# Kernel tuning notes

Hardware: AMD Instinct MI355X
Metric: run time of the kernel (lower is better)

Reference implementation:

```python
import jax, jax.numpy as jnp
import numpy as np

N_PER_GRAPH = 1024
BATCH = 32
N = N_PER_GRAPH * BATCH  # 32768 total nodes
E = 262144               # edges per edge set (before self loops)
EMB = 128
D = 128
NEG_SLOPE = 0.2


def setup_inputs() -> dict:
    key = jax.random.key(0)
    ks = jax.random.split(key, 20)
    def lin(k, i, o):
        return (jax.random.normal(k, (i, o), jnp.float32) / np.float32(np.sqrt(i)))
    inp = {}
    inp["x"] = jax.random.normal(ks[0], (N, EMB), jnp.float32)
    inp["edge_index_n"] = jax.random.randint(ks[1], (2, E), 0, N, jnp.int32)
    inp["edge_index_r0"] = jax.random.randint(ks[2], (2, E), 0, N, jnp.int32)
    inp["edge_index_r1"] = jax.random.randint(ks[3], (2, E), 0, N, jnp.int32)
    # gat_0: Linear(EMB->D) + attn Linear(2D->D)
    inp["W0_lin"] = lin(ks[4], EMB, D); inp["b0_lin"] = jnp.zeros((D,), jnp.float32)
    inp["W0_att"] = lin(ks[5], 2 * D, D); inp["b0_att"] = jnp.zeros((D,), jnp.float32)
    # gat_1 (shared, used twice)
    inp["W1_lin"] = lin(ks[6], D, D); inp["b1_lin"] = jnp.zeros((D,), jnp.float32)
    inp["W1_att"] = lin(ks[7], 2 * D, D); inp["b1_att"] = jnp.zeros((D,), jnp.float32)
    # gat_2 (shared, used twice)
    inp["W2_lin"] = lin(ks[8], D, D); inp["b2_lin"] = jnp.zeros((D,), jnp.float32)
    inp["W2_att"] = lin(ks[9], 2 * D, D); inp["b2_att"] = jnp.zeros((D,), jnp.float32)
    # lin_prob: Linear(D->1)
    inp["Wp"] = lin(ks[10], D, 1); inp["bp"] = jnp.zeros((1,), jnp.float32)
    # Attention: W1, W2 (D->D, no bias), vt (D->1, no bias)
    inp["Wa1"] = lin(ks[11], D, D)
    inp["Wa2"] = lin(ks[12], D, D)
    inp["vt"] = lin(ks[13], D, 1)
    return inp


def _gat(x, edge_index, Wl, bl, Wa, ba):
    """One GATConv: add self loops, lin, edge gather, attn MLP, segment softmax, scatter-add."""
    n = x.shape[0]
    loop = jnp.arange(n, dtype=edge_index.dtype)
    src = jnp.concatenate([edge_index[0], loop])  # x_j index
    dst = jnp.concatenate([edge_index[1], loop])  # x_i / aggregation index
    h = x @ Wl + bl                               # [N, D]
    hi = h[dst]                                   # [E+N, D]
    hj = h[src]                                   # [E+N, D]
    a = jnp.concatenate([hi, hj], axis=-1) @ Wa + ba  # [E+N, D]
    a = jax.nn.leaky_relu(a, NEG_SLOPE)
    # segment softmax over destination neighborhoods (vector-valued, per channel)
    m = jax.lax.stop_gradient(jax.ops.segment_max(a, dst, num_segments=n))
    ex = jnp.exp(a - m[dst])
    s = jax.ops.segment_sum(ex, dst, num_segments=n)
    alpha = ex / (s[dst] + 1e-16)
    return jax.ops.segment_sum(hj * alpha, dst, num_segments=n)


def reference(x, edge_index_n, edge_index_r0, edge_index_r1,
              W0_lin, b0_lin, W0_att, b0_att,
              W1_lin, b1_lin, W1_att, b1_att,
              W2_lin, b2_lin, W2_att, b2_att,
              Wp, bp, Wa1, Wa2, vt):
    g0 = _gat(x,  edge_index_n,  W0_lin, b0_lin, W0_att, b0_att)
    g1 = _gat(g0, edge_index_r1, W1_lin, b1_lin, W1_att, b1_att)
    g2 = _gat(g1, edge_index_r0, W2_lin, b2_lin, W2_att, b2_att)
    g3 = _gat(g2, edge_index_r1, W1_lin, b1_lin, W1_att, b1_att)
    g4 = _gat(g3, edge_index_r0, W2_lin, b2_lin, W2_att, b2_att)
    X = g4.reshape(BATCH, N_PER_GRAPH, D)
    h = X.mean(axis=1)                                       # [B, D]
    logits1 = (X @ Wp + bp).reshape(BATCH, N_PER_GRAPH)      # [B, n]
    prob1 = jax.nn.softmax(logits1[:, 1:], axis=-1)          # [B, n-1]
    k1, k2 = jax.random.split(jax.random.key(42))
    index1 = 1 + jax.random.categorical(k1, logits1[:, 1:], axis=-1)  # [B]
    b_ar = jnp.arange(BATCH)
    sampled = X[b_ar, index1][:, None, :]                    # [B, 1, D]
    u = (jnp.tanh(sampled @ Wa1 + X @ Wa2) @ vt)[..., 0]      # [B, n]
    u = u.at[b_ar, index1].set(-jnp.inf)
    prob2 = jax.nn.softmax(u[:, 1:], axis=-1)                # [B, n-1]
    index2 = 1 + jax.random.categorical(k2, u[:, 1:], axis=-1)
    probs = prob1[b_ar, index1 - 1] + prob2[b_ar, index2 - 1]
    log_probs = jnp.log(probs)
    return (h, index1, index2, log_probs)
```

## Files before the change

kernel.cpp:

```cpp
#include <hip/hip_runtime.h>
#include <stdint.h>
#include <math.h>

#define NN 32768
#define EE 262144
#define DD 128
#define NPG 1024
#define NB 32
#define NEG_SLOPE 0.2f
#define USE_PARTITIONABLE 1

__host__ __device__ inline void tf2x32(uint32_t k0, uint32_t k1, uint32_t c0, uint32_t c1,
                                       uint32_t* o0, uint32_t* o1) {
  uint32_t ks2 = k0 ^ k1 ^ 0x1BD11BDAu;
  uint32_t x0 = c0 + k0;
  uint32_t x1 = c1 + k1;
#define TFR(r) { x0 += x1; x1 = (x1 << (r)) | (x1 >> (32 - (r))); x1 ^= x0; }
  TFR(13) TFR(15) TFR(26) TFR(6)
  x0 += k1; x1 += ks2 + 1u;
  TFR(17) TFR(29) TFR(16) TFR(24)
  x0 += ks2; x1 += k0 + 2u;
  TFR(13) TFR(15) TFR(26) TFR(6)
  x0 += k0; x1 += k1 + 3u;
  TFR(17) TFR(29) TFR(16) TFR(24)
  x0 += k1; x1 += ks2 + 4u;
  TFR(13) TFR(15) TFR(26) TFR(6)
  x0 += ks2; x1 += k0 + 5u;
#undef TFR
  *o0 = x0; *o1 = x1;
}

__device__ inline float gumbel_from_bits(uint32_t bits) {
  float fl = __uint_as_float((bits >> 9) | 0x3f800000u) - 1.0f;
  const float tiny = 1.17549435e-38f;
  float u = fmaxf(tiny, fl + tiny);
  return -logf(-logf(u));
}

__device__ inline float gumbel_at(uint32_t ka, uint32_t kb, uint32_t f) {
#if USE_PARTITIONABLE
  uint32_t o0, o1;
  tf2x32(ka, kb, 0u, f, &o0, &o1);
  return gumbel_from_bits(o0 ^ o1);
#else
  const uint32_t HALF = 16368u;
  uint32_t o0, o1;
  if (f < HALF) { tf2x32(ka, kb, f, f + HALF, &o0, &o1); return gumbel_from_bits(o0); }
  else          { tf2x32(ka, kb, f - HALF, f, &o0, &o1); return gumbel_from_bits(o1); }
#endif
}

__global__ __launch_bounds__(256) void hist_kernel(const int* __restrict__ dst,
                                                   int* __restrict__ counts) {
  int i = blockIdx.x * 256 + threadIdx.x;
  atomicAdd(&counts[dst[i]], 1);
}

__global__ __launch_bounds__(1024) void scan_kernel(const int* __restrict__ counts,
                                                    int* __restrict__ rowptr,
                                                    int* __restrict__ cursor) {
  __shared__ int part[1024];
  int t = threadIdx.x;
  int base = t * 32;
  int local[32];
  {
    const int4* c4 = (const int4*)(counts + base);
    int s = 0;
#pragma unroll
    for (int v = 0; v < 8; v++) {
      int4 cc = c4[v];
      local[v * 4 + 0] = s; s += cc.x;
      local[v * 4 + 1] = s; s += cc.y;
      local[v * 4 + 2] = s; s += cc.z;
      local[v * 4 + 3] = s; s += cc.w;
    }
    part[t] = s;
  }
  __syncthreads();
  int own = part[t];
  int run = own;
  for (int off = 1; off < 1024; off <<= 1) {
    int v = (t >= off) ? part[t - off] : 0;
    __syncthreads();
    part[t] += v;
    __syncthreads();
  }
  (void)run;
  int excl = part[t] - own;
  {
    int4* rp4 = (int4*)(rowptr + base);
    int4* cu4 = (int4*)(cursor + base);
#pragma unroll
    for (int v = 0; v < 8; v++) {
      int4 w;
      w.x = excl + local[v * 4 + 0];
      w.y = excl + local[v * 4 + 1];
      w.z = excl + local[v * 4 + 2];
      w.w = excl + local[v * 4 + 3];
      rp4[v] = w;
      cu4[v] = w;
    }
  }
  if (t == 1023) rowptr[NN] = part[1023];
}

__global__ __launch_bounds__(256) void scatter_kernel(const int* __restrict__ src,
                                                      const int* __restrict__ dst,
                                                      int* __restrict__ cursor,
                                                      int* __restrict__ col) {
  int i = blockIdx.x * 256 + threadIdx.x;
  int p = atomicAdd(&cursor[dst[i]], 1);
  col[p] = src[i];
}

__global__ __launch_bounds__(256) void gemm128_kernel(const float* __restrict__ in,
                                                      const float* __restrict__ W,
                                                      const float* __restrict__ bias,
                                                      float* __restrict__ out, int hasBias) {
  __shared__ __align__(16) float ws[128 * 128];
  __shared__ __align__(16) float ins[64][132];
  int t = threadIdx.x;
  size_t row0 = (size_t)blockIdx.x * 64;
  {
    const float4* W4 = (const float4*)W;
    float4* ws4 = (float4*)ws;
#pragma unroll
    for (int i = 0; i < 16; i++) ws4[t + 256 * i] = W4[t + 256 * i];
    const float4* in4 = (const float4*)(in + row0 * 128);
#pragma unroll
    for (int i = 0; i < 8; i++) {
      int idx = t + 256 * i;
      int r = idx >> 5, c4 = idx & 31;
      float4 v = in4[(size_t)r * 32 + c4];
      *(float4*)&ins[r][c4 * 4] = v;
    }
  }
  __syncthreads();
  int cg = t & 15, rg = t >> 4;
  int c0 = cg * 8, r0 = rg * 4;
  float acc[4][8] = {};
#pragma unroll 8
  for (int k = 0; k < 128; k++) {
    float4 wA = *(const float4*)&ws[k * 128 + c0];
    float4 wB = *(const float4*)&ws[k * 128 + c0 + 4];
    float av[4];
    av[0] = ins[r0 + 0][k]; av[1] = ins[r0 + 1][k];
    av[2] = ins[r0 + 2][k]; av[3] = ins[r0 + 3][k];
#pragma unroll
    for (int i = 0; i < 4; i++) {
      acc[i][0] += av[i] * wA.x; acc[i][1] += av[i] * wA.y;
      acc[i][2] += av[i] * wA.z; acc[i][3] += av[i] * wA.w;
      acc[i][4] += av[i] * wB.x; acc[i][5] += av[i] * wB.y;
      acc[i][6] += av[i] * wB.z; acc[i][7] += av[i] * wB.w;
    }
  }
  float bb[8];
#pragma unroll
  for (int j = 0; j < 8; j++) bb[j] = hasBias ? bias[c0 + j] : 0.0f;
#pragma unroll
  for (int i = 0; i < 4; i++) {
    float* orow = out + (row0 + r0 + i) * 128 + c0;
    float4 o0, o1;
    o0.x = acc[i][0] + bb[0]; o0.y = acc[i][1] + bb[1];
    o0.z = acc[i][2] + bb[2]; o0.w = acc[i][3] + bb[3];
    o1.x = acc[i][4] + bb[4]; o1.y = acc[i][5] + bb[5];
    o1.z = acc[i][6] + bb[6]; o1.w = acc[i][7] + bb[7];
    *(float4*)orow = o0;
    *(float4*)(orow + 4) = o1;
  }
}

__device__ inline float lk1(float v) { return v > 0.f ? v : NEG_SLOPE * v; }

__global__ __launch_bounds__(256, 4) void gat_edge_kernel(const float* __restrict__ P,
                                                          const float* __restrict__ Q,
                                                          const float* __restrict__ H,
                                                          const int* __restrict__ rowptr,
                                                          const int* __restrict__ col,
                                                          float* __restrict__ out) {
  int wv = threadIdx.x >> 6;
  int lane = threadIdx.x & 63;
  int dst = (blockIdx.x << 2) + wv;
  int rs = __builtin_amdgcn_readfirstlane(rowptr[dst]);
  int re = __builtin_amdgcn_readfirstlane(rowptr[dst + 1]);
  int deg = re - rs;
  int total = deg + 1;
  float2 pd = ((const float2*)(P + (size_t)dst * DD))[lane];

  float mx = -INFINITY, my = -INFINITY;
  float sx = 0.f, sy = 0.f;
  float cx = 0.f, cy = 0.f;

  for (int base = 0; base < total; base += 64) {
    int cnt = min(64, total - base);
    int e = base + lane;
    int myidx = (e < deg) ? col[rs + e] : dst;
    int i = 0;
    for (; i + 4 <= cnt; i += 4) {
      int iu = __builtin_amdgcn_readfirstlane(i);
      int n0 = __builtin_amdgcn_readlane(myidx, iu);
      int n1 = __builtin_amdgcn_readlane(myidx, iu + 1);
      int n2 = __builtin_amdgcn_readlane(myidx, iu + 2);
      int n3 = __builtin_amdgcn_readlane(myidx, iu + 3);
      float2 q0 = ((const float2*)(Q + (size_t)n0 * DD))[lane];
      float2 q1 = ((const float2*)(Q + (size_t)n1 * DD))[lane];
      float2 q2 = ((const float2*)(Q + (size_t)n2 * DD))[lane];
      float2 q3 = ((const float2*)(Q + (size_t)n3 * DD))[lane];
      float2 h0 = ((const float2*)(H + (size_t)n0 * DD))[lane];
      float2 h1 = ((const float2*)(H + (size_t)n1 * DD))[lane];
      float2 h2 = ((const float2*)(H + (size_t)n2 * DD))[lane];
      float2 h3 = ((const float2*)(H + (size_t)n3 * DD))[lane];
      float a0x = lk1(pd.x + q0.x), a0y = lk1(pd.y + q0.y);
      float a1x = lk1(pd.x + q1.x), a1y = lk1(pd.y + q1.y);
      float a2x = lk1(pd.x + q2.x), a2y = lk1(pd.y + q2.y);
      float a3x = lk1(pd.x + q3.x), a3y = lk1(pd.y + q3.y);
      float nmx = fmaxf(fmaxf(mx, fmaxf(a0x, a1x)), fmaxf(a2x, a3x));
      float nmy = fmaxf(fmaxf(my, fmaxf(a0y, a1y)), fmaxf(a2y, a3y));
      float scx = expf(mx - nmx), scy = expf(my - nmy);
      float e0x = expf(a0x - nmx), e1x = expf(a1x - nmx);
      float e2x = expf(a2x - nmx), e3x = expf(a3x - nmx);
      float e0y = expf(a0y - nmy), e1y = expf(a1y - nmy);
      float e2y = expf(a2y - nmy), e3y = expf(a3y - nmy);
      sx = sx * scx + ((e0x + e1x) + (e2x + e3x));
      sy = sy * scy + ((e0y + e1y) + (e2y + e3y));
      cx = cx * scx + ((e0x * h0.x + e1x * h1.x) + (e2x * h2.x + e3x * h3.x));
      cy = cy * scy + ((e0y * h0.y + e1y * h1.y) + (e2y * h2.y + e3y * h3.y));
      mx = nmx; my = nmy;
    }
    for (; i < cnt; i++) {
      int iu = __builtin_amdgcn_readfirstlane(i);
      int n0 = __builtin_amdgcn_readlane(myidx, iu);
      float2 q0 = ((const float2*)(Q + (size_t)n0 * DD))[lane];
      float2 h0 = ((const float2*)(H + (size_t)n0 * DD))[lane];
      float a0x = lk1(pd.x + q0.x), a0y = lk1(pd.y + q0.y);
      float nmx = fmaxf(mx, a0x), nmy = fmaxf(my, a0y);
      float scx = expf(mx - nmx), scy = expf(my - nmy);
      float e0x = expf(a0x - nmx), e0y = expf(a0y - nmy);
      sx = sx * scx + e0x;
      sy = sy * scy + e0y;
      cx = cx * scx + e0x * h0.x;
      cy = cy * scy + e0y * h0.y;
      mx = nmx; my = nmy;
    }
  }
  float2 o = make_float2(cx / (sx + 1e-16f), cy / (sy + 1e-16f));
  ((float2*)(out + (size_t)dst * DD))[lane] = o;
}

__global__ __launch_bounds__(256) void logits_kernel(const float* __restrict__ X,
                                                     const float* __restrict__ Wp,
                                                     const float* __restrict__ bp,
                                                     float* __restrict__ logits) {
  int w = threadIdx.x >> 6, lane = threadIdx.x & 63;
  int n = blockIdx.x * 4 + w;
  const float* xr = X + (size_t)n * DD;
  float p = xr[lane] * Wp[lane] + xr[lane + 64] * Wp[lane + 64];
  for (int off = 32; off > 0; off >>= 1) p += __shfl_down(p, off);
  if (lane == 0) logits[n] = p + bp[0];
}

__global__ __launch_bounds__(1024) void hmean_kernel(const float* __restrict__ X,
                                                     float* __restrict__ out) {
  int b = blockIdx.x;
  int t = threadIdx.x;
  int c = t & 127, part = t >> 7;
  float acc = 0.f;
  for (int i = part; i < NPG; i += 8)
    acc += X[((size_t)b * NPG + i) * DD + c];
  __shared__ float red[1024];
  red[t] = acc; __syncthreads();
  if (part == 0) {
    float s = 0.f;
#pragma unroll
    for (int p = 0; p < 8; p++) s += red[p * 128 + c];
    out[b * DD + c] = s * (1.0f / (float)NPG);
  }
}

__global__ __launch_bounds__(256) void sample1_kernel(const float* __restrict__ logits,
                                                      uint32_t ka, uint32_t kb,
                                                      int* __restrict__ idx1_ws,
                                                      float* __restrict__ p1_ws,
                                                      float* __restrict__ out) {
  int b = blockIdx.x, t = threadIdx.x;
  __shared__ float sV[256]; __shared__ int sJ[256]; __shared__ float sM[256];
  float bestV = -INFINITY; int bestJ = 1 << 30; float maxL = -INFINITY;
  for (int j = 1 + t; j < NPG; j += 256) {
    float l = logits[(size_t)b * NPG + j];
    maxL = fmaxf(maxL, l);
    float v = l + gumbel_at(ka, kb, (uint32_t)(b * 1023 + j - 1));
    if (v > bestV) { bestV = v; bestJ = j; }
  }
  sV[t] = bestV; sJ[t] = bestJ; sM[t] = maxL; __syncthreads();
  for (int off = 128; off > 0; off >>= 1) {
    if (t < off) {
      if (sV[t + off] > sV[t] || (sV[t + off] == sV[t] && sJ[t + off] < sJ[t])) {
        sV[t] = sV[t + off]; sJ[t] = sJ[t + off];
      }
      sM[t] = fmaxf(sM[t], sM[t + off]);
    }
    __syncthreads();
  }
  float M = sM[0]; int idx = sJ[0];
  __syncthreads();
  float ps = 0.f;
  for (int j = 1 + t; j < NPG; j += 256)
    ps += expf(logits[(size_t)b * NPG + j] - M);
  sV[t] = ps; __syncthreads();
  for (int off = 128; off > 0; off >>= 1) {
    if (t < off) sV[t] += sV[t + off];
    __syncthreads();
  }
  if (t == 0) {
    float S = sV[0];
    float p1 = expf(logits[(size_t)b * NPG + idx] - M) / S;
    idx1_ws[b] = idx;
    p1_ws[b] = p1;
    out[NB * DD + b] = (float)idx;
  }
}

__global__ __launch_bounds__(128) void zk_kernel(const float* __restrict__ X,
                                                 const float* __restrict__ Wa1,
                                                 const int* __restrict__ idx1,
                                                 float* __restrict__ Z) {
  int b = blockIdx.x, c = threadIdx.x;
  __shared__ float xs[128];
  int node = b * NPG + idx1[b];
  xs[c] = X[(size_t)node * DD + c];
  __syncthreads();
  float acc = 0.f;
#pragma unroll 8
  for (int k = 0; k < 128; k++) acc += xs[k] * Wa1[k * 128 + c];
  Z[b * DD + c] = acc;
}

__global__ __launch_bounds__(256) void u_kernel(const float* __restrict__ Y,
                                                const float* __restrict__ Z,
                                                const float* __restrict__ vt,
                                                const int* __restrict__ idx1,
                                                float* __restrict__ u) {
  int w = threadIdx.x >> 6, lane = threadIdx.x & 63;
  int n = blockIdx.x * 4 + w;
  int b = n >> 10;
  float t0 = tanhf(Z[b * DD + lane] + Y[(size_t)n * DD + lane]) * vt[lane];
  float t1 = tanhf(Z[b * DD + lane + 64] + Y[(size_t)n * DD + lane + 64]) * vt[lane + 64];
  float p = t0 + t1;
  for (int off = 32; off > 0; off >>= 1) p += __shfl_down(p, off);
  if (lane == 0) u[n] = ((n & (NPG - 1)) == idx1[b]) ? -INFINITY : p;
}

__global__ __launch_bounds__(256) void sample2_kernel(const float* __restrict__ u,
                                                      uint32_t ka, uint32_t kb,
                                                      const float* __restrict__ p1_ws,
                                                      float* __restrict__ out) {
  int b = blockIdx.x, t = threadIdx.x;
  __shared__ float sV[256]; __shared__ int sJ[256]; __shared__ float sM[256];
  float bestV = -INFINITY; int bestJ = 1 << 30; float maxL = -INFINITY;
  for (int j = 1 + t; j < NPG; j += 256) {
    float l = u[(size_t)b * NPG + j];
    maxL = fmaxf(maxL, l);
    float v = l + gumbel_at(ka, kb, (uint32_t)(b * 1023 + j - 1));
    if (v > bestV) { bestV = v; bestJ = j; }
  }
  sV[t] = bestV; sJ[t] = bestJ; sM[t] = maxL; __syncthreads();
  for (int off = 128; off > 0; off >>= 1) {
    if (t < off) {
      if (sV[t + off] > sV[t] || (sV[t + off] == sV[t] && sJ[t + off] < sJ[t])) {
        sV[t] = sV[t + off]; sJ[t] = sJ[t + off];
      }
      sM[t] = fmaxf(sM[t], sM[t + off]);
    }
    __syncthreads();
  }
  float M = sM[0]; int idx = sJ[0];
  __syncthreads();
  float ps = 0.f;
  for (int j = 1 + t; j < NPG; j += 256) {
    float l = u[(size_t)b * NPG + j];
    ps += expf(l - M);
  }
  sV[t] = ps; __syncthreads();
  for (int off = 128; off > 0; off >>= 1) {
    if (t < off) sV[t] += sV[t + off];
    __syncthreads();
  }
  if (t == 0) {
    float S = sV[0];
    float p2 = expf(u[(size_t)b * NPG + idx] - M) / S;
    out[NB * DD + NB + b] = (float)idx;
    out[NB * DD + 2 * NB + b] = logf(p1_ws[b] + p2);
  }
}

extern "C" void kernel_launch(void* const* d_in, const int* in_sizes, int n_in,
                              void* d_out, int out_size, void* d_ws, size_t ws_size,
                              hipStream_t stream) {
  const float* x  = (const float*)d_in[0];
  const int* eN   = (const int*)d_in[1];
  const int* eR0  = (const int*)d_in[2];
  const int* eR1  = (const int*)d_in[3];
  const float* W0l = (const float*)d_in[4];  const float* b0l = (const float*)d_in[5];
  const float* W0a = (const float*)d_in[6];  const float* b0a = (const float*)d_in[7];
  const float* W1l = (const float*)d_in[8];  const float* b1l = (const float*)d_in[9];
  const float* W1a = (const float*)d_in[10]; const float* b1a = (const float*)d_in[11];
  const float* W2l = (const float*)d_in[12]; const float* b2l = (const float*)d_in[13];
  const float* W2a = (const float*)d_in[14]; const float* b2a = (const float*)d_in[15];
  const float* Wp  = (const float*)d_in[16]; const float* bp  = (const float*)d_in[17];
  const float* Wa1 = (const float*)d_in[18]; const float* Wa2 = (const float*)d_in[19];
  const float* vt  = (const float*)d_in[20];
  float* out = (float*)d_out;

  char* wsb = (char*)d_ws;
  size_t off = 0;
  auto take = [&](size_t bytes) -> char* {
    char* p = wsb + off;
    off += (bytes + 255) & ~(size_t)255;
    return p;
  };
  int* rowptrAll = (int*)take((size_t)3 * (NN + 1) * sizeof(int));
  int* counts    = (int*)take((size_t)NN * sizeof(int));
  int* cursor    = (int*)take((size_t)NN * sizeof(int));
  int* colAll    = (int*)take((size_t)3 * EE * sizeof(int));
  float* bufA    = (float*)take((size_t)NN * DD * 4);
  float* bufB    = (float*)take((size_t)NN * DD * 4);
  float* hb      = (float*)take((size_t)NN * DD * 4);
  float* Pb      = (float*)take((size_t)NN * DD * 4);
  float* Qb      = (float*)take((size_t)NN * DD * 4);
  float* logits  = (float*)take((size_t)NN * 4);
  float* ub      = (float*)take((size_t)NN * 4);
  float* Zb      = (float*)take((size_t)NB * DD * 4);
  int* idx1b     = (int*)take(NB * 4);
  float* p1b     = (float*)take(NB * 4);

  uint32_t k1a, k1b, k2a, k2b;
#if USE_PARTITIONABLE
  {
    uint32_t o0, o1;
    tf2x32(0u, 42u, 0u, 0u, &o0, &o1); k1a = o0; k1b = o1;
    tf2x32(0u, 42u, 0u, 1u, &o0, &o1); k2a = o0; k2b = o1;
  }
#else
  {
    uint32_t a0, b0, a1, b1;
    tf2x32(0u, 42u, 0u, 2u, &a0, &b0);
    tf2x32(0u, 42u, 1u, 3u, &a1, &b1);
    k1a = a0; k1b = a1; k2a = b0; k2b = b1;
  }
#endif

  const int* esets[3] = {eN, eR0, eR1};
  for (int s = 0; s < 3; s++) {
    int* rp = rowptrAll + s * (NN + 1);
    int* cl = colAll + (size_t)s * EE;
    hipMemsetAsync(counts, 0, NN * sizeof(int), stream);
    hist_kernel<<<EE / 256, 256, 0, stream>>>(esets[s] + EE, counts);
    scan_kernel<<<1, 1024, 0, stream>>>(counts, rp, cursor);
    scatter_kernel<<<EE / 256, 256, 0, stream>>>(esets[s], esets[s] + EE, cursor, cl);
  }

  struct Layer { const float* in; float* o; const float *Wl, *bl, *Wa, *ba; int set; };
  Layer Ls[5] = {
      {x,    bufA, W0l, b0l, W0a, b0a, 0},
      {bufA, bufB, W1l, b1l, W1a, b1a, 2},
      {bufB, bufA, W2l, b2l, W2a, b2a, 1},
      {bufA, bufB, W1l, b1l, W1a, b1a, 2},
      {bufB, bufA, W2l, b2l, W2a, b2a, 1},
  };
  for (int L = 0; L < 5; L++) {
    gemm128_kernel<<<NN / 64, 256, 0, stream>>>(Ls[L].in, Ls[L].Wl, Ls[L].bl, hb, 1);
    gemm128_kernel<<<NN / 64, 256, 0, stream>>>(hb, Ls[L].Wa, Ls[L].ba, Pb, 1);
    gemm128_kernel<<<NN / 64, 256, 0, stream>>>(hb, Ls[L].Wa + 128 * 128, nullptr, Qb, 0);
    gat_edge_kernel<<<NN / 4, 256, 0, stream>>>(
        Pb, Qb, hb, rowptrAll + Ls[L].set * (NN + 1),
        colAll + (size_t)Ls[L].set * EE, Ls[L].o);
  }
  const float* X = bufA;

  gemm128_kernel<<<NN / 64, 256, 0, stream>>>(X, Wa2, nullptr, Pb, 0);
  logits_kernel<<<NN / 4, 256, 0, stream>>>(X, Wp, bp, logits);
  hmean_kernel<<<NB, 1024, 0, stream>>>(X, out);
  sample1_kernel<<<NB, 256, 0, stream>>>(logits, k1a, k1b, idx1b, p1b, out);
  zk_kernel<<<NB, 128, 0, stream>>>(X, Wa1, idx1b, Zb);
  u_kernel<<<NN / 4, 256, 0, stream>>>(Pb, Zb, vt, idx1b, ub);
  sample2_kernel<<<NB, 256, 0, stream>>>(ub, k2a, k2b, p1b, out);
}
```

Measured before the change: 902.7 us.

## Fuse per-layer GEMMs into one kernel and batch CSR build across edge sets

Replaces the three per-layer GEMM launches (h = xWl, P, Q) with one kernel that keeps the 128-row input tile and the intermediate h tile in shared memory, transposed, and reuses them for all three products with an 8x8 register tile per thread. It also merges the three edge sets' histogram, scan and scatter into single launches over concatenated buffers. This removes the re-reads of h from global memory and cuts kernel launches. In exchange the fused kernel uses about 130 KB of LDS with launch bounds of one block, so occupancy drops to one block per CU, and grid size falls to 256 blocks.

```diff
diff --git a/kernel.cpp b/kernel.cpp
--- a/kernel.cpp
+++ b/kernel.cpp
@@ -8,6 +8,7 @@
 #define NPG 1024
 #define NB 32
 #define NEG_SLOPE 0.2f
+#define ATP 132
 #define USE_PARTITIONABLE 1
 
 __host__ __device__ inline void tf2x32(uint32_t k0, uint32_t k1, uint32_t c0, uint32_t c1,
@@ -50,42 +51,48 @@
 #endif
 }
 
-__global__ __launch_bounds__(256) void hist_kernel(const int* __restrict__ dst,
-                                                   int* __restrict__ counts) {
-  int i = blockIdx.x * 256 + threadIdx.x;
-  atomicAdd(&counts[dst[i]], 1);
-}
-
-__global__ __launch_bounds__(1024) void scan_kernel(const int* __restrict__ counts,
-                                                    int* __restrict__ rowptr,
-                                                    int* __restrict__ cursor) {
+__global__ __launch_bounds__(256) void hist3_kernel(const int* __restrict__ e0,
+                                                    const int* __restrict__ e1,
+                                                    const int* __restrict__ e2,
+                                                    int* __restrict__ counts3) {
+  int s = blockIdx.x >> 10;
+  int i = (blockIdx.x & 1023) * 256 + threadIdx.x;
+  const int* d = (s == 0) ? e0 : (s == 1) ? e1 : e2;
+  atomicAdd(&counts3[s * NN + d[i + EE]], 1);
+}
+
+__global__ __launch_bounds__(1024) void scan3_kernel(const int* __restrict__ counts3,
+                                                     int* __restrict__ rowptrAll,
+                                                     int* __restrict__ cursorAll) {
   __shared__ int part[1024];
+  int s = blockIdx.x;
+  const int* counts = counts3 + s * NN;
+  int* rowptr = rowptrAll + s * (NN + 1);
+  int* cursor = cursorAll + s * NN;
   int t = threadIdx.x;
   int base = t * 32;
   int local[32];
   {
     const int4* c4 = (const int4*)(counts + base);
-    int s = 0;
+    int sum = 0;
 #pragma unroll
     for (int v = 0; v < 8; v++) {
       int4 cc = c4[v];
-      local[v * 4 + 0] = s; s += cc.x;
-      local[v * 4 + 1] = s; s += cc.y;
-      local[v * 4 + 2] = s; s += cc.z;
-      local[v * 4 + 3] = s; s += cc.w;
-    }
-    part[t] = s;
+      local[v * 4 + 0] = sum; sum += cc.x;
+      local[v * 4 + 1] = sum; sum += cc.y;
+      local[v * 4 + 2] = sum; sum += cc.z;
+      local[v * 4 + 3] = sum; sum += cc.w;
+    }
+    part[t] = sum;
   }
   __syncthreads();
   int own = part[t];
-  int run = own;
   for (int off = 1; off < 1024; off <<= 1) {
     int v = (t >= off) ? part[t - off] : 0;
     __syncthreads();
     part[t] += v;
     __syncthreads();
   }
-  (void)run;
   int excl = part[t] - own;
   {
     int4* rp4 = (int4*)(rowptr + base);
@@ -104,13 +111,17 @@
   if (t == 1023) rowptr[NN] = part[1023];
 }
 
-__global__ __launch_bounds__(256) void scatter_kernel(const int* __restrict__ src,
-                                                      const int* __restrict__ dst,
-                                                      int* __restrict__ cursor,
-                                                      int* __restrict__ col) {
-  int i = blockIdx.x * 256 + threadIdx.x;
-  int p = atomicAdd(&cursor[dst[i]], 1);
-  col[p] = src[i];
+__global__ __launch_bounds__(256) void scatter3_kernel(const int* __restrict__ e0,
+                                                       const int* __restrict__ e1,
+                                                       const int* __restrict__ e2,
+                                                       int* __restrict__ cursorAll,
+                                                       int* __restrict__ colAll) {
+  int s = blockIdx.x >> 10;
+  int i = (blockIdx.x & 1023) * 256 + threadIdx.x;
+  const int* e = (s == 0) ? e0 : (s == 1) ? e1 : e2;
+  int src = e[i], dst = e[i + EE];
+  int p = atomicAdd(&cursorAll[s * NN + dst], 1);
+  colAll[(size_t)s * EE + p] = src;
 }
 
 __global__ __launch_bounds__(256) void gemm128_kernel(const float* __restrict__ in,
@@ -168,6 +179,111 @@
     *(float4*)orow = o0;
     *(float4*)(orow + 4) = o1;
   }
+}
+
+__global__ __launch_bounds__(256, 1) void fused_layer_kernel(
+    const float* __restrict__ in, const float* __restrict__ Wl,
+    const float* __restrict__ bl, const float* __restrict__ Wa,
+    const float* __restrict__ ba, float* __restrict__ h,
+    float* __restrict__ P, float* __restrict__ Q) {
+  __shared__ __align__(16) float at[128 * ATP];
+  __shared__ __align__(16) float ws[128 * 128];
+  int t = threadIdx.x;
+  size_t row0 = (size_t)blockIdx.x * 128;
+  int tr = t >> 4, tc = t & 15;
+  int r0 = tr * 8, c0 = tc * 8;
+  float acc[8][8];
+
+  auto stage_ws = [&](const float* src) {
+    const float4* s4 = (const float4*)src;
+    float4* d4 = (float4*)ws;
+#pragma unroll
+    for (int i = 0; i < 16; i++) d4[t + 256 * i] = s4[t + 256 * i];
+  };
+  auto transpose_ws_to_at = [&]() {
+#pragma unroll
+    for (int i = 0; i < 16; i++) {
+      int idx = t + 256 * i;
+      int k = idx & 127;
+      int rg = idx >> 7;
+      float4 v;
+      v.x = ws[(rg * 4 + 0) * 128 + k];
+      v.y = ws[(rg * 4 + 1) * 128 + k];
+      v.z = ws[(rg * 4 + 2) * 128 + k];
+      v.w = ws[(rg * 4 + 3) * 128 + k];
+      *(float4*)&at[k * ATP + rg * 4] = v;
+    }
+  };
+  auto mm = [&](const float* bias) {
+#pragma unroll
+    for (int i = 0; i < 8; i++)
+#pragma unroll
+      for (int j = 0; j < 8; j++) acc[i][j] = 0.f;
+#pragma unroll 2
+    for (int k = 0; k < 128; k++) {
+      float4 a0 = *(const float4*)&at[k * ATP + r0];
+      float4 a1 = *(const float4*)&at[k * ATP + r0 + 4];
+      float4 w0 = *(const float4*)&ws[k * 128 + c0];
+      float4 w1 = *(const float4*)&ws[k * 128 + c0 + 4];
+      float av[8] = {a0.x, a0.y, a0.z, a0.w, a1.x, a1.y, a1.z, a1.w};
+      float wv[8] = {w0.x, w0.y, w0.z, w0.w, w1.x, w1.y, w1.z, w1.w};
+#pragma unroll
+      for (int i = 0; i < 8; i++)
+#pragma unroll
+        for (int j = 0; j < 8; j++) acc[i][j] += av[i] * wv[j];
+    }
+    if (bias) {
+#pragma unroll
+      for (int j = 0; j < 8; j++) {
+        float b = bias[c0 + j];
+#pragma unroll
+        for (int i = 0; i < 8; i++) acc[i][j] += b;
+      }
+    }
+  };
+  auto writeout = [&](float* dst) {
+#pragma unroll
+    for (int i = 0; i < 8; i++) {
+      float* orow = dst + (row0 + r0 + i) * DD + c0;
+      float4 o0, o1;
+      o0.x = acc[i][0]; o0.y = acc[i][1]; o0.z = acc[i][2]; o0.w = acc[i][3];
+      o1.x = acc[i][4]; o1.y = acc[i][5]; o1.z = acc[i][6]; o1.w = acc[i][7];
+      *(float4*)orow = o0;
+      *(float4*)(orow + 4) = o1;
+    }
+  };
+
+  stage_ws(in + row0 * DD);
+  __syncthreads();
+  transpose_ws_to_at();
+  __syncthreads();
+  stage_ws(Wl);
+  __syncthreads();
+  mm(bl);
+  writeout(h);
+  __syncthreads();
+  {
+#pragma unroll
+    for (int i = 0; i < 8; i++) {
+      float4 o0, o1;
+      o0.x = acc[i][0]; o0.y = acc[i][1]; o0.z = acc[i][2]; o0.w = acc[i][3];
+      o1.x = acc[i][4]; o1.y = acc[i][5]; o1.z = acc[i][6]; o1.w = acc[i][7];
+      *(float4*)&ws[(r0 + i) * 128 + c0] = o0;
+      *(float4*)&ws[(r0 + i) * 128 + c0 + 4] = o1;
+    }
+  }
+  __syncthreads();
+  transpose_ws_to_at();
+  __syncthreads();
+  stage_ws(Wa);
+  __syncthreads();
+  mm(ba);
+  writeout(P);
+  __syncthreads();
+  stage_ws(Wa + 128 * 128);
+  __syncthreads();
+  mm(nullptr);
+  writeout(Q);
 }
 
 __device__ inline float lk1(float v) { return v > 0.f ? v : NEG_SLOPE * v; }
@@ -419,8 +535,8 @@
     return p;
   };
   int* rowptrAll = (int*)take((size_t)3 * (NN + 1) * sizeof(int));
-  int* counts    = (int*)take((size_t)NN * sizeof(int));
-  int* cursor    = (int*)take((size_t)NN * sizeof(int));
+  int* counts3   = (int*)take((size_t)3 * NN * sizeof(int));
+  int* cursorAll = (int*)take((size_t)3 * NN * sizeof(int));
   int* colAll    = (int*)take((size_t)3 * EE * sizeof(int));
   float* bufA    = (float*)take((size_t)NN * DD * 4);
   float* bufB    = (float*)take((size_t)NN * DD * 4);
@@ -449,15 +565,10 @@
   }
 #endif
 
-  const int* esets[3] = {eN, eR0, eR1};
-  for (int s = 0; s < 3; s++) {
-    int* rp = rowptrAll + s * (NN + 1);
-    int* cl = colAll + (size_t)s * EE;
-    hipMemsetAsync(counts, 0, NN * sizeof(int), stream);
-    hist_kernel<<<EE / 256, 256, 0, stream>>>(esets[s] + EE, counts);
-    scan_kernel<<<1, 1024, 0, stream>>>(counts, rp, cursor);
-    scatter_kernel<<<EE / 256, 256, 0, stream>>>(esets[s], esets[s] + EE, cursor, cl);
-  }
+  hipMemsetAsync(counts3, 0, (size_t)3 * NN * sizeof(int), stream);
+  hist3_kernel<<<3 * 1024, 256, 0, stream>>>(eN, eR0, eR1, counts3);
+  scan3_kernel<<<3, 1024, 0, stream>>>(counts3, rowptrAll, cursorAll);
+  scatter3_kernel<<<3 * 1024, 256, 0, stream>>>(eN, eR0, eR1, cursorAll, colAll);
 
   struct Layer { const float* in; float* o; const float *Wl, *bl, *Wa, *ba; int set; };
   Layer Ls[5] = {
@@ -468,9 +579,8 @@
       {bufB, bufA, W2l, b2l, W2a, b2a, 1},
   };
   for (int L = 0; L < 5; L++) {
-    gemm128_kernel<<<NN / 64, 256, 0, stream>>>(Ls[L].in, Ls[L].Wl, Ls[L].bl, hb, 1);
-    gemm128_kernel<<<NN / 64, 256, 0, stream>>>(hb, Ls[L].Wa, Ls[L].ba, Pb, 1);
-    gemm128_kernel<<<NN / 64, 256, 0, stream>>>(hb, Ls[L].Wa + 128 * 128, nullptr, Qb, 0);
+    fused_layer_kernel<<<NN / 128, 256, 0, stream>>>(
+        Ls[L].in, Ls[L].Wl, Ls[L].bl, Ls[L].Wa, Ls[L].ba, hb, Pb, Qb);
     gat_edge_kernel<<<NN / 4, 256, 0, stream>>>(
         Pb, Qb, hb, rowptrAll + Ls[L].set * (NN + 1),
         colAll + (size_t)Ls[L].set * EE, Ls[L].o);
```

Measured after the change: 788.7 us. -12.6%, faster.

## Rewrite GEMM as double-buffered 128x128 tile kernel and batch CSR builds

Applied to the files above, without the earlier changes.

Replaces the 128-wide GEMM, which staged the whole weight matrix in LDS for 64-row tiles, with a kernel that computes 128-row tiles. It streams K in 16-wide chunks through double-buffered LDS and gives each thread an 8x8 register tile. The three per-edge-set CSR construction passes (memset, histogram, scan, scatter) are merged into single launches covering all three sets. This cuts launch count and LDS footprint and raises arithmetic intensity per LDS load, at the cost of more registers per thread. The transposed A stores into LDS may also cause bank conflicts.

```diff
diff --git a/kernel.cpp b/kernel.cpp
--- a/kernel.cpp
+++ b/kernel.cpp
@@ -50,42 +50,48 @@
 #endif
 }
 
-__global__ __launch_bounds__(256) void hist_kernel(const int* __restrict__ dst,
-                                                   int* __restrict__ counts) {
-  int i = blockIdx.x * 256 + threadIdx.x;
-  atomicAdd(&counts[dst[i]], 1);
-}
-
-__global__ __launch_bounds__(1024) void scan_kernel(const int* __restrict__ counts,
-                                                    int* __restrict__ rowptr,
-                                                    int* __restrict__ cursor) {
+__global__ __launch_bounds__(256) void hist3_kernel(const int* __restrict__ e0,
+                                                    const int* __restrict__ e1,
+                                                    const int* __restrict__ e2,
+                                                    int* __restrict__ counts3) {
+  int s = blockIdx.x >> 10;
+  int i = (blockIdx.x & 1023) * 256 + threadIdx.x;
+  const int* d = (s == 0) ? e0 : (s == 1) ? e1 : e2;
+  atomicAdd(&counts3[s * NN + d[i + EE]], 1);
+}
+
+__global__ __launch_bounds__(1024) void scan3_kernel(const int* __restrict__ counts3,
+                                                     int* __restrict__ rowptrAll,
+                                                     int* __restrict__ cursorAll) {
   __shared__ int part[1024];
+  int s = blockIdx.x;
+  const int* counts = counts3 + s * NN;
+  int* rowptr = rowptrAll + s * (NN + 1);
+  int* cursor = cursorAll + s * NN;
   int t = threadIdx.x;
   int base = t * 32;
   int local[32];
   {
     const int4* c4 = (const int4*)(counts + base);
-    int s = 0;
+    int sum = 0;
 #pragma unroll
     for (int v = 0; v < 8; v++) {
       int4 cc = c4[v];
-      local[v * 4 + 0] = s; s += cc.x;
-      local[v * 4 + 1] = s; s += cc.y;
-      local[v * 4 + 2] = s; s += cc.z;
-      local[v * 4 + 3] = s; s += cc.w;
-    }
-    part[t] = s;
+      local[v * 4 + 0] = sum; sum += cc.x;
+      local[v * 4 + 1] = sum; sum += cc.y;
+      local[v * 4 + 2] = sum; sum += cc.z;
+      local[v * 4 + 3] = sum; sum += cc.w;
+    }
+    part[t] = sum;
   }
   __syncthreads();
   int own = part[t];
-  int run = own;
   for (int off = 1; off < 1024; off <<= 1) {
     int v = (t >= off) ? part[t - off] : 0;
     __syncthreads();
     part[t] += v;
     __syncthreads();
   }
-  (void)run;
   int excl = part[t] - own;
   {
     int4* rp4 = (int4*)(rowptr + base);
@@ -104,69 +110,103 @@
   if (t == 1023) rowptr[NN] = part[1023];
 }
 
-__global__ __launch_bounds__(256) void scatter_kernel(const int* __restrict__ src,
-                                                      const int* __restrict__ dst,
-                                                      int* __restrict__ cursor,
-                                                      int* __restrict__ col) {
-  int i = blockIdx.x * 256 + threadIdx.x;
-  int p = atomicAdd(&cursor[dst[i]], 1);
-  col[p] = src[i];
-}
-
-__global__ __launch_bounds__(256) void gemm128_kernel(const float* __restrict__ in,
-                                                      const float* __restrict__ W,
-                                                      const float* __restrict__ bias,
-                                                      float* __restrict__ out, int hasBias) {
-  __shared__ __align__(16) float ws[128 * 128];
-  __shared__ __align__(16) float ins[64][132];
+__global__ __launch_bounds__(256) void scatter3_kernel(const int* __restrict__ e0,
+                                                       const int* __restrict__ e1,
+                                                       const int* __restrict__ e2,
+                                                       int* __restrict__ cursorAll,
+                                                       int* __restrict__ colAll) {
+  int s = blockIdx.x >> 10;
+  int i = (blockIdx.x & 1023) * 256 + threadIdx.x;
+  const int* e = (s == 0) ? e0 : (s == 1) ? e1 : e2;
+  int src = e[i], dst = e[i + EE];
+  int p = atomicAdd(&cursorAll[s * NN + dst], 1);
+  colAll[(size_t)s * EE + p] = src;
+}
+
+#define FMA4(ac, s, v) { ac.x += (s) * (v).x; ac.y += (s) * (v).y; \
+                         ac.z += (s) * (v).z; ac.w += (s) * (v).w; }
+
+__global__ __launch_bounds__(256, 2) void gemm8_kernel(const float* __restrict__ in,
+                                                       const float* __restrict__ W,
+                                                       const float* __restrict__ bias,
+                                                       float* __restrict__ out) {
+  __shared__ __align__(16) float at[2][16 * 132];
+  __shared__ __align__(16) float ws[2][16 * 128];
   int t = threadIdx.x;
-  size_t row0 = (size_t)blockIdx.x * 64;
-  {
-    const float4* W4 = (const float4*)W;
-    float4* ws4 = (float4*)ws;
-#pragma unroll
-    for (int i = 0; i < 16; i++) ws4[t + 256 * i] = W4[t + 256 * i];
-    const float4* in4 = (const float4*)(in + row0 * 128);
-#pragma unroll
-    for (int i = 0; i < 8; i++) {
-      int idx = t + 256 * i;
-      int r = idx >> 5, c4 = idx & 31;
-      float4 v = in4[(size_t)r * 32 + c4];
-      *(float4*)&ins[r][c4 * 4] = v;
-    }
-  }
+  size_t row0 = (size_t)blockIdx.x * 128;
+  int tr = t >> 4, tcg = t & 15;
+  int r0 = tr * 8;
+  float4 acc0[8], acc1[8];
+#pragma unroll
+  for (int i = 0; i < 8; i++) {
+    acc0[i] = make_float4(0.f, 0.f, 0.f, 0.f);
+    acc1[i] = make_float4(0.f, 0.f, 0.f, 0.f);
+  }
+  int srow = t >> 2;
+  int sc4 = (t & 3) * 4;
+  int kkA = t >> 5;
+  int jgA = (t & 31) * 4;
+
+  float4 a0, a1, w0, w1;
+  auto load_chunk = [&](int k0) {
+    a0 = *(const float4*)&in[(row0 + srow) * DD + k0 + sc4];
+    a1 = *(const float4*)&in[(row0 + srow + 64) * DD + k0 + sc4];
+    w0 = *(const float4*)&W[(size_t)(k0 + kkA) * DD + jgA];
+    w1 = *(const float4*)&W[(size_t)(k0 + kkA + 8) * DD + jgA];
+  };
+  auto write_chunk = [&](int b) {
+    float* A = at[b];
+    A[(sc4 + 0) * 132 + srow] = a0.x;
+    A[(sc4 + 1) * 132 + srow] = a0.y;
+    A[(sc4 + 2) * 132 + srow] = a0.z;
+    A[(sc4 + 3) * 132 + srow] = a0.w;
+    A[(sc4 + 0) * 132 + srow + 64] = a1.x;
+    A[(sc4 + 1) * 132 + srow + 64] = a1.y;
+    A[(sc4 + 2) * 132 + srow + 64] = a1.z;
+    A[(sc4 + 3) * 132 + srow + 64] = a1.w;
+    float* Wd = ws[b];
+    *(float4*)&Wd[kkA * 128 + jgA] = w0;
+    *(float4*)&Wd[(kkA + 8) * 128 + jgA] = w1;
+  };
+
+  load_chunk(0);
+  write_chunk(0);
   __syncthreads();
-  int cg = t & 15, rg = t >> 4;
-  int c0 = cg * 8, r0 = rg * 4;
-  float acc[4][8] = {};
-#pragma unroll 8
-  for (int k = 0; k < 128; k++) {
-    float4 wA = *(const float4*)&ws[k * 128 + c0];
-    float4 wB = *(const float4*)&ws[k * 128 + c0 + 4];
-    float av[4];
-    av[0] = ins[r0 + 0][k]; av[1] = ins[r0 + 1][k];
-    av[2] = ins[r0 + 2][k]; av[3] = ins[r0 + 3][k];
-#pragma unroll
-    for (int i = 0; i < 4; i++) {
-      acc[i][0] += av[i] * wA.x; acc[i][1] += av[i] * wA.y;
-      acc[i][2] += av[i] * wA.z; acc[i][3] += av[i] * wA.w;
-      acc[i][4] += av[i] * wB.x; acc[i][5] += av[i] * wB.y;
-      acc[i][6] += av[i] * wB.z; acc[i][7] += av[i] * wB.w;
-    }
-  }
-  float bb[8];
-#pragma unroll
-  for (int j = 0; j < 8; j++) bb[j] = hasBias ? bias[c0 + j] : 0.0f;
-#pragma unroll
-  for (int i = 0; i < 4; i++) {
-    float* orow = out + (row0 + r0 + i) * 128 + c0;
-    float4 o0, o1;
-    o0.x = acc[i][0] + bb[0]; o0.y = acc[i][1] + bb[1];
-    o0.z = acc[i][2] + bb[2]; o0.w = acc[i][3] + bb[3];
-    o1.x = acc[i][4] + bb[4]; o1.y = acc[i][5] + bb[5];
-    o1.z = acc[i][6] + bb[6]; o1.w = acc[i][7] + bb[7];
-    *(float4*)orow = o0;
-    *(float4*)(orow + 4) = o1;
+  for (int kc = 0; kc < 8; ++kc) {
+    int cur = kc & 1;
+    if (kc < 7) load_chunk((kc + 1) * 16);
+    const float* A = at[cur];
+    const float* Wd = ws[cur];
+#pragma unroll
+    for (int kk = 0; kk < 16; ++kk) {
+      float4 av0 = *(const float4*)&A[kk * 132 + r0];
+      float4 av1 = *(const float4*)&A[kk * 132 + r0 + 4];
+      float4 wv0 = *(const float4*)&Wd[kk * 128 + 4 * tcg];
+      float4 wv1 = *(const float4*)&Wd[kk * 128 + 4 * tcg + 64];
+      float as[8] = {av0.x, av0.y, av0.z, av0.w, av1.x, av1.y, av1.z, av1.w};
+#pragma unroll
+      for (int i = 0; i < 8; i++) {
+        FMA4(acc0[i], as[i], wv0);
+        FMA4(acc1[i], as[i], wv1);
+      }
+    }
+    if (kc < 7) {
+      write_chunk(cur ^ 1);
+    }
+    __syncthreads();
+  }
+  float4 b0 = make_float4(0.f, 0.f, 0.f, 0.f), b1 = b0;
+  if (bias) {
+    b0 = *(const float4*)&bias[4 * tcg];
+    b1 = *(const float4*)&bias[4 * tcg + 64];
+  }
+#pragma unroll
+  for (int i = 0; i < 8; i++) {
+    float4 o0 = acc0[i], o1 = acc1[i];
+    o0.x += b0.x; o0.y += b0.y; o0.z += b0.z; o0.w += b0.w;
+    o1.x += b1.x; o1.y += b1.y; o1.z += b1.z; o1.w += b1.w;
+    *(float4*)&out[(row0 + r0 + i) * DD + 4 * tcg] = o0;
+    *(float4*)&out[(row0 + r0 + i) * DD + 4 * tcg + 64] = o1;
   }
 }
 
@@ -419,8 +459,8 @@
     return p;
   };
   int* rowptrAll = (int*)take((size_t)3 * (NN + 1) * sizeof(int));
-  int* counts    = (int*)take((size_t)NN * sizeof(int));
-  int* cursor    = (int*)take((size_t)NN * sizeof(int));
+  int* counts3   = (int*)take((size_t)3 * NN * sizeof(int));
+  int* cursorAll = (int*)take((size_t)3 * NN * sizeof(int));
   int* colAll    = (int*)take((size_t)3 * EE * sizeof(int));
   float* bufA    = (float*)take((size_t)NN * DD * 4);
   float* bufB    = (float*)take((size_t)NN * DD * 4);
@@ -449,15 +489,10 @@
   }
 #endif
 
-  const int* esets[3] = {eN, eR0, eR1};
-  for (int s = 0; s < 3; s++) {
-    int* rp = rowptrAll + s * (NN + 1);
-    int* cl = colAll + (size_t)s * EE;
-    hipMemsetAsync(counts, 0, NN * sizeof(int), stream);
-    hist_kernel<<<EE / 256, 256, 0, stream>>>(esets[s] + EE, counts);
-    scan_kernel<<<1, 1024, 0, stream>>>(counts, rp, cursor);
-    scatter_kernel<<<EE / 256, 256, 0, stream>>>(esets[s], esets[s] + EE, cursor, cl);
-  }
+  hipMemsetAsync(counts3, 0, (size_t)3 * NN * sizeof(int), stream);
+  hist3_kernel<<<3 * 1024, 256, 0, stream>>>(eN, eR0, eR1, counts3);
+  scan3_kernel<<<3, 1024, 0, stream>>>(counts3, rowptrAll, cursorAll);
+  scatter3_kernel<<<3 * 1024, 256, 0, stream>>>(eN, eR0, eR1, cursorAll, colAll);
 
   struct Layer { const float* in; float* o; const float *Wl, *bl, *Wa, *ba; int set; };
   Layer Ls[5] = {
@@ -468,16 +503,16 @@
       {bufB, bufA, W2l, b2l, W2a, b2a, 1},
   };
   for (int L = 0; L < 5; L++) {
-    gemm128_kernel<<<NN / 64, 256, 0, stream>>>(Ls[L].in, Ls[L].Wl, Ls[L].bl, hb, 1);
-    gemm128_kernel<<<NN / 64, 256, 0, stream>>>(hb, Ls[L].Wa, Ls[L].ba, Pb, 1);
-    gemm128_kernel<<<NN / 64, 256, 0, stream>>>(hb, Ls[L].Wa + 128 * 128, nullptr, Qb, 0);
+    gemm8_kernel<<<NN / 128, 256, 0, stream>>>(Ls[L].in, Ls[L].Wl, Ls[L].bl, hb);
+    gemm8_kernel<<<NN / 128, 256, 0, stream>>>(hb, Ls[L].Wa, Ls[L].ba, Pb);
+    gemm8_kernel<<<NN / 128, 256, 0, stream>>>(hb, Ls[L].Wa + 128 * 128, nullptr, Qb);
     gat_edge_kernel<<<NN / 4, 256, 0, stream>>>(
         Pb, Qb, hb, rowptrAll + Ls[L].set * (NN + 1),
         colAll + (size_t)Ls[L].set * EE, Ls[L].o);
   }
   const float* X = bufA;
 
-  gemm128_kernel<<<NN / 64, 256, 0, stream>>>(X, Wa2, nullptr, Pb, 0);
+  gemm8_kernel<<<NN / 128, 256, 0, stream>>>(X, Wa2, nullptr, Pb);
   logits_kernel<<<NN / 4, 256, 0, stream>>>(X, Wp, bp, logits);
   hmean_kernel<<<NB, 1024, 0, stream>>>(X, out);
   sample1_kernel<<<NB, 256, 0, stream>>>(logits, k1a, k1b, idx1b, p1b, out);
```

New measurement: 1.721 ms. +90.7%, slower.
